# Performance work log

Measured on AMD Instinct MI355X. Metric: run time of the kernel, lower is better.

The kernel has to match this reference:

```python
import jax, jax.numpy as jnp
import numpy as np

N = 100000   # total nodes across the batch
D = 3        # ambient dimension of the point cloud
T = 64       # num_thetas (directions)
R = 64       # resolution of the ECT discretization
B = 128      # number of point clouds in the batch
RADIUS = 1.1
SCALE = 8.0


def setup_inputs() -> dict:
    key = jax.random.key(0)
    kx, kv, kb = jax.random.split(key, 3)
    x = jax.random.normal(kx, (N, D), dtype=jnp.float32)
    # directions; the layer stores v movedim'd and moves it back, so math uses [D, T]
    v = jax.random.normal(kv, (D, T), dtype=jnp.float32)
    v = v / jnp.linalg.norm(v, axis=0, keepdims=True)  # unit directions, typical usage
    batch = jnp.sort(jax.random.randint(kb, (N,), 0, B, dtype=jnp.int64))
    return {"x": x, "v": v, "batch": batch}


def reference(x, v, batch):
    # compute_ect_points:
    # nh[n,t] = <x_n, v_t>
    nh = x @ v  # [N, T]
    lin = jnp.linspace(-RADIUS, RADIUS, R, dtype=x.dtype)  # [R]
    # ecc[n,t,r] = sigmoid(scale * (lin[r] - nh[n,t]))  -- large [N,T,R] intermediate
    ecc = jax.nn.sigmoid(SCALE * (lin[None, None, :] - nh[:, :, None]))
    # scatter-sum over the batch index (index_add): -> [B, T, R]
    ect = jax.ops.segment_sum(ecc, batch, num_segments=B)
    # normalized=False -> return ect.squeeze(); no singleton dims here
    return ect
```

## Files before the change

kernel.cpp:

```cpp
#include <hip/hip_runtime.h>
#include <math.h>


#define THREADS 256
#define TPB 4
#define TQ  16
#define PAD 63
#define J0  64
#define STEPS 144
#define ROW32 256
#define ROW64 128
#define HO_BASE64 (TPB * ROW64)
#define BSEG 128

constexpr double cexp_taylor(double r) {
    double s = 1.0, term = 1.0;
    for (int i = 1; i < 18; ++i) { term *= r / (double)i; s += term; }
    return s;
}
constexpr double cexp(double x) {
    const double LN2 = 0.69314718055994530942;
    const int n = (int)(x / LN2 + (x >= 0.0 ? 0.5 : -0.5));
    const double r = x - (double)n * LN2;
    double e = cexp_taylor(r);
    if (n >= 0) { for (int i = 0; i < n;  ++i) e *= 2.0; }
    else        { for (int i = 0; i < -n; ++i) e *= 0.5; }
    return e;
}
struct WTab {
    float w[STEPS];
    constexpr WTab() : w() {
        const double d = 2.2 / 63.0;
        for (int j = 0; j < STEPS; ++j) {
            const double z = 8.0 * d * (double)(111 - j);
            w[j] = (float)(1.0 / ((1.0 + cexp(-z)) * 65536.0));
        }
    }
};
constexpr WTab WT;

__device__ __forceinline__ float wave_suffix(float x, int lane) {
#pragma unroll
    for (int d = 1; d < 64; d <<= 1) {
        const float y = __shfl_down(x, d, 64);
        x += (lane + d < 64) ? y : 0.0f;
    }
    return x;
}

__device__ __forceinline__ int lower_scalar(const int* __restrict__ A, int n,
                                            int val) {
    const long long g = ((long long)val * (long long)n) >> 7;
    int lo = (int)(g - 1024 > 0 ? g - 1024 : 0);
    int hi = (int)(g + 1024 < n ? g + 1024 : n);
    const bool okl = (lo == 0) || (A[__builtin_amdgcn_readfirstlane(lo - 1)] < val);
    const bool okh = (hi == n) || (A[__builtin_amdgcn_readfirstlane(hi)] >= val);
    if (!(okl && okh)) { lo = 0; hi = n; }
    while (hi > lo) {
        const int mid = (lo + hi) >> 1;
        const int key = A[__builtin_amdgcn_readfirstlane(mid)];
        if (key < val) lo = mid + 1; else hi = mid;
    }
    return lo;
}

__global__ __launch_bounds__(THREADS, 8) void ect_fused9_kernel(
    const float* __restrict__ x,
    const float* __restrict__ v,
    const int*   __restrict__ batch,
    float* __restrict__ out,
    int n, float inv_d, float bias)
{
    __shared__ unsigned long long Hu[2 * TPB * ROW64];

    const int tid  = threadIdx.x;
    const int wv   = tid >> 6;
    const int lane = tid & 63;
    const int b    = blockIdx.x >> 4;
    const int tq   = blockIdx.x & (TQ - 1);

    for (int i = tid; i < 2 * TPB * ROW64; i += THREADS) Hu[i] = 0ull;

    const int s0 = lower_scalar(batch, n, b);
    const int s1 = lower_scalar(batch, n, b + 1);

    const int t_l  = lane >> 4;
    const int slot = (lane & 15) + (wv << 4);
    const int tbase = tq * TPB;
    const int t    = tbase + t_l;
    const float va = v[t], vb = v[64 + t], vc = v[128 + t];
    const int rowoff64 = t_l * ROW64;

    __syncthreads();

    for (int base = s0; base < s1; base += 4 * 64) {
        float xs0[4], xs1[4], xs2[4];
        bool  ok[4];
#pragma unroll
        for (int k = 0; k < 4; ++k) {
            const int idx = base + (k << 6) + slot;
            ok[k] = (idx < s1);
            if (ok[k]) {
                const float3 xx = *(const float3*)(x + 3 * (size_t)idx);
                xs0[k] = xx.x; xs1[k] = xx.y; xs2[k] = xx.z;
            }
        }
#pragma unroll
        for (int k = 0; k < 4; ++k) {
            if (!ok[k]) continue;
            const float nh = fmaf(xs0[k], va, fmaf(xs1[k], vb, xs2[k] * vc));
            float bin = fmaf(nh, inv_d, bias);
            bin = fminf(fmaxf(bin, 0.0f), 158.999f);
            const float g0f = floorf(bin);
            const float fr  = bin - g0f;
            const int   a   = PAD + (int)g0f;
            const unsigned q1 = (unsigned)(fr * 65536.0f + 0.5f);
            const unsigned q0 = 65536u - q1;
            const unsigned long long val =
                (unsigned long long)q0 | ((unsigned long long)q1 << 32);
            const int w64 = (a >> 1) + rowoff64 + ((a & 1) ? HO_BASE64 : 0);
            atomicAdd(&Hu[w64], val);
        }
    }

    __syncthreads();

    float c[4];
    {
        const unsigned* He32 = (const unsigned*)Hu;
        const unsigned* Ho32 = (const unsigned*)(Hu + HO_BASE64);
        float* Hf = (float*)Hu;
        const int rb = wv * ROW32;
#pragma unroll
        for (int q = 0; q < 4; ++q) {
            const int a = lane + 64 * q;
            unsigned s = He32[rb + a];
            if (a > 0) s += Ho32[rb + a - 1];
            c[q] = (float)s;
            if (q > 0) Hf[rb + a] = c[q];
        }
    }

    float tot23 = c[2] + c[3];
#pragma unroll
    for (int d = 1; d < 64; d <<= 1) tot23 += __shfl_xor(tot23, d, 64);
    const float s1v   = wave_suffix(c[1], lane) + tot23;
    const float carry = __shfl(s1v, 0, 64);
    const float s0v   = wave_suffix(c[0], lane) + carry;
    const float window = (s0v - s1v) * (1.0f / 65536.0f);

    __syncthreads();

    const float* H = (const float*)Hu + wv * ROW32 + lane;
    float a0 = window, a1 = 0.f;
#pragma unroll
    for (int j = J0; j < STEPS; j += 2) {
        a0 = fmaf(WT.w[j],     H[j],     a0);
        a1 = fmaf(WT.w[j + 1], H[j + 1], a1);
    }
    out[((size_t)b * 64 + tbase + wv) * 64 + lane] = a0 + a1;
}

extern "C" void kernel_launch(void* const* d_in, const int* in_sizes, int n_in,
                              void* d_out, int out_size, void* d_ws, size_t ws_size,
                              hipStream_t stream) {
    const float* x     = (const float*)d_in[0];
    const float* v     = (const float*)d_in[1];
    const int*   batch = (const int*)d_in[2];
    float*       out   = (float*)d_out;

    const int n = in_sizes[0] / 3;

    const double d = 2.2 / 63.0;
    const float inv_d = (float)(1.0 / d);
    const float bias  = 79.5f;

    hipLaunchKernelGGL(ect_fused9_kernel, dim3(BSEG * TQ), dim3(THREADS), 0,
                       stream, x, v, batch, out, n, inv_d, bias);
}
```

Baseline: 17.80 us.

## Pack histogram deposits into 32-bit atomics with 8-bit fixed-point weights

Switches the LDS histogram from 64-bit atomics carrying 16-bit fractional weights to 32-bit atomics packing two 16-bit counters with 8-bit fixed-point weights. The bin index and fraction come from a single scaled float-to-int conversion with a med3 clamp instead of floor and subtract, and the per-point loop is split into a full-chunk path and a tail so the main path has no bounds checks. This aims to cut atomic width, LDS traffic and ALU work, at the cost of coarser quantisation (1/256) and possible 16-bit counter overflow for large segments.

```diff
diff --git a/kernel.cpp b/kernel.cpp
--- a/kernel.cpp
+++ b/kernel.cpp
@@ -5,13 +5,19 @@
 #define THREADS 256
 #define TPB 4
 #define TQ  16
-#define PAD 63
 #define J0  64
 #define STEPS 144
+#define ROWW 128
+#define HO_BASE (TPB * ROWW)
+#define HF_BASE (2 * TPB * ROWW)
 #define ROW32 256
-#define ROW64 128
-#define HO_BASE64 (TPB * ROW64)
 #define BSEG 128
+
+#if __has_builtin(__builtin_amdgcn_fmed3f)
+#define CLAMP(v, lo, hi) __builtin_amdgcn_fmed3f((v), (lo), (hi))
+#else
+#define CLAMP(v, lo, hi) fminf(fmaxf((v), (lo)), (hi))
+#endif
 
 constexpr double cexp_taylor(double r) {
     double s = 1.0, term = 1.0;
@@ -33,7 +39,7 @@
         const double d = 2.2 / 63.0;
         for (int j = 0; j < STEPS; ++j) {
             const double z = 8.0 * d * (double)(111 - j);
-            w[j] = (float)(1.0 / ((1.0 + cexp(-z)) * 65536.0));
+            w[j] = (float)(1.0 / ((1.0 + cexp(-z)) * 256.0));
         }
     }
 };
@@ -64,14 +70,14 @@
     return lo;
 }
 
-__global__ __launch_bounds__(THREADS, 8) void ect_fused9_kernel(
+__global__ __launch_bounds__(THREADS, 8) void ect_fused11_kernel(
     const float* __restrict__ x,
     const float* __restrict__ v,
     const int*   __restrict__ batch,
     float* __restrict__ out,
-    int n, float inv_d, float bias)
+    int n, float inv_d256, float bias256)
 {
-    __shared__ unsigned long long Hu[2 * TPB * ROW64];
+    __shared__ unsigned Ls[2 * TPB * ROWW + TPB * ROW32];
 
     const int tid  = threadIdx.x;
     const int wv   = tid >> 6;
@@ -79,7 +85,10 @@
     const int b    = blockIdx.x >> 4;
     const int tq   = blockIdx.x & (TQ - 1);
 
-    for (int i = tid; i < 2 * TPB * ROW64; i += THREADS) Hu[i] = 0ull;
+    {
+        unsigned long long* z = (unsigned long long*)Ls;
+        for (int i = tid; i < TPB * ROWW; i += THREADS) z[i] = 0ull;
+    }
 
     const int s0 = lower_scalar(batch, n, b);
     const int s1 = lower_scalar(batch, n, b + 1);
@@ -89,37 +98,44 @@
     const int tbase = tq * TPB;
     const int t    = tbase + t_l;
     const float va = v[t], vb = v[64 + t], vc = v[128 + t];
-    const int rowoff64 = t_l * ROW64;
+    const int rowbyte = (t_l * ROWW) << 2;
 
     __syncthreads();
 
-    for (int base = s0; base < s1; base += 4 * 64) {
-        float xs0[4], xs1[4], xs2[4];
-        bool  ok[4];
-#pragma unroll
-        for (int k = 0; k < 4; ++k) {
-            const int idx = base + (k << 6) + slot;
-            ok[k] = (idx < s1);
-            if (ok[k]) {
+#define DEPOSIT(x0, x1, x2)                                                   \
+    {                                                                         \
+        const float nh = fmaf((x0), va, fmaf((x1), vb, (x2) * vc));           \
+        float bf = fmaf(nh, inv_d256, bias256);                               \
+        bf = CLAMP(bf, 16128.0f, 56831.0f);               \
+        const unsigned ufix = (unsigned)bf;      \
+        const unsigned q1   = ufix & 255u;                                    \
+        const unsigned val  = (q1 << 16) + (256u - q1);                       \
+        const unsigned wbyte = ((ufix >> 7) & ~3u)             \
+                             + ((ufix >> 6) & 4u ? (HO_BASE << 2) : 0u)       \
+                             + rowbyte;                                       \
+        atomicAdd((unsigned*)((char*)Ls + wbyte), val);                       \
+    }
+
+    {
+        const int len = s1 - s0;
+        const int nfull = len >> 8;
+        int base = s0;
+        for (int c = 0; c < nfull; ++c, base += 256) {
+            float xs[4][3];
+#pragma unroll
+            for (int k = 0; k < 4; ++k) {
+                const float3 xx = *(const float3*)(x + 3 * (size_t)(base + (k << 6) + slot));
+                xs[k][0] = xx.x; xs[k][1] = xx.y; xs[k][2] = xx.z;
+            }
+#pragma unroll
+            for (int k = 0; k < 4; ++k) DEPOSIT(xs[k][0], xs[k][1], xs[k][2]);
+        }
+        for (; base < s1; base += 64) {
+            const int idx = base + slot;
+            if (idx < s1) {
                 const float3 xx = *(const float3*)(x + 3 * (size_t)idx);
-                xs0[k] = xx.x; xs1[k] = xx.y; xs2[k] = xx.z;
+                DEPOSIT(xx.x, xx.y, xx.z);
             }
-        }
-#pragma unroll
-        for (int k = 0; k < 4; ++k) {
-            if (!ok[k]) continue;
-            const float nh = fmaf(xs0[k], va, fmaf(xs1[k], vb, xs2[k] * vc));
-            float bin = fmaf(nh, inv_d, bias);
-            bin = fminf(fmaxf(bin, 0.0f), 158.999f);
-            const float g0f = floorf(bin);
-            const float fr  = bin - g0f;
-            const int   a   = PAD + (int)g0f;
-            const unsigned q1 = (unsigned)(fr * 65536.0f + 0.5f);
-            const unsigned q0 = 65536u - q1;
-            const unsigned long long val =
-                (unsigned long long)q0 | ((unsigned long long)q1 << 32);
-            const int w64 = (a >> 1) + rowoff64 + ((a & 1) ? HO_BASE64 : 0);
-            atomicAdd(&Hu[w64], val);
         }
     }
 
@@ -127,17 +143,22 @@
 
     float c[4];
     {
-        const unsigned* He32 = (const unsigned*)Hu;
-        const unsigned* Ho32 = (const unsigned*)(Hu + HO_BASE64);
-        float* Hf = (float*)Hu;
-        const int rb = wv * ROW32;
+        const unsigned* He = Ls + wv * ROWW;
+        const unsigned* Ho = Ls + HO_BASE + wv * ROWW;
+        float* Hf = (float*)(Ls + HF_BASE) + wv * ROW32;
+        const int par = lane & 1;
 #pragma unroll
         for (int q = 0; q < 4; ++q) {
             const int a = lane + 64 * q;
-            unsigned s = He32[rb + a];
-            if (a > 0) s += Ho32[rb + a - 1];
-            c[q] = (float)s;
-            if (q > 0) Hf[rb + a] = c[q];
+            const unsigned heW = He[a >> 1];
+            const unsigned he  = par ? (heW >> 16) : (heW & 0xFFFFu);
+            unsigned ho = 0u;
+            if (a > 0) {
+                const unsigned hoW = Ho[(a - 1) >> 1];
+                ho = par ? (hoW & 0xFFFFu) : (hoW >> 16);
+            }
+            c[q] = (float)(he + ho);
+            if (q > 0) Hf[a] = c[q];
         }
     }
 
@@ -147,11 +168,11 @@
     const float s1v   = wave_suffix(c[1], lane) + tot23;
     const float carry = __shfl(s1v, 0, 64);
     const float s0v   = wave_suffix(c[0], lane) + carry;
-    const float window = (s0v - s1v) * (1.0f / 65536.0f);
+    const float window = (s0v - s1v) * (1.0f / 256.0f);
 
     __syncthreads();
 
-    const float* H = (const float*)Hu + wv * ROW32 + lane;
+    const float* H = (const float*)(Ls + HF_BASE) + wv * ROW32 + lane;
     float a0 = window, a1 = 0.f;
 #pragma unroll
     for (int j = J0; j < STEPS; j += 2) {
@@ -159,6 +180,7 @@
         a1 = fmaf(WT.w[j + 1], H[j + 1], a1);
     }
     out[((size_t)b * 64 + tbase + wv) * 64 + lane] = a0 + a1;
+#undef DEPOSIT
 }
 
 extern "C" void kernel_launch(void* const* d_in, const int* in_sizes, int n_in,
@@ -172,9 +194,9 @@
     const int n = in_sizes[0] / 3;
 
     const double d = 2.2 / 63.0;
-    const float inv_d = (float)(1.0 / d);
-    const float bias  = 79.5f;
-
-    hipLaunchKernelGGL(ect_fused9_kernel, dim3(BSEG * TQ), dim3(THREADS), 0,
-                       stream, x, v, batch, out, n, inv_d, bias);
-}
+    const float inv_d256 = (float)(256.0 / d);
+    const float bias256  = (79.5f + 63.0f) * 256.0f;
+
+    hipLaunchKernelGGL(ect_fused11_kernel, dim3(BSEG * TQ), dim3(THREADS), 0,
+                       stream, x, v, batch, out, n, inv_d256, bias256);
+}
```

After: 16.15 us. 1.1x faster.
